# Kernel tuning notes

Measured on AMD Instinct MI355X. Metric: run time of the kernel, lower is better.

The kernel has to match this reference:

```python
import jax, jax.numpy as jnp
import numpy as np

N0, N1, N2 = 200000, 50000, 10000
D_IN, D_PROMPT, D_HID, D_OUT = 128, 64, 256, 2
E0, E1 = 800000, 160000


def _glorot(key, shape):
    fan_in, fan_out = shape[0], shape[1]
    lim = np.sqrt(6.0 / (fan_in + fan_out))
    return jax.random.uniform(key, shape, jnp.float32, -lim, lim)


def setup_inputs() -> dict:
    key = jax.random.key(0)
    ks = jax.random.split(key, 20)
    inp = {
        "features": jax.random.normal(ks[0], (N0, D_IN), jnp.float32),
        "membership_mask": jax.random.randint(ks[1], (N0,), 0, 2) > 0,
        "src0": jax.random.randint(ks[2], (E0,), 0, N0),
        "dst0": jax.random.randint(ks[3], (E0,), 0, N1),
        "src1": jax.random.randint(ks[4], (E1,), 0, N1),
        "dst1": jax.random.randint(ks[5], (E1,), 0, N2),
        "output_nodes_indices": jax.random.randint(ks[6], (N2,), 0, N2),
        # prompt MLPs
        "w_pin": _glorot(ks[7], (D_IN, D_PROMPT)),
        "b_pin": jnp.zeros((D_PROMPT,), jnp.float32),
        "w_pout": _glorot(ks[8], (D_IN, D_PROMPT)),
        "b_pout": jnp.zeros((D_PROMPT,), jnp.float32),
        # SAGEConv layer 0: (D_IN+D_PROMPT) -> D_HID
        "w_self0": _glorot(ks[9], (D_IN + D_PROMPT, D_HID)),
        "w_neigh0": _glorot(ks[10], (D_IN + D_PROMPT, D_HID)),
        "b0": jnp.zeros((D_HID,), jnp.float32),
        # SAGEConv layer 1: D_HID -> D_HID
        "w_self1": _glorot(ks[11], (D_HID, D_HID)),
        "w_neigh1": _glorot(ks[12], (D_HID, D_HID)),
        "b1": jnp.zeros((D_HID,), jnp.float32),
        # classifier
        "w_cls": _glorot(ks[13], (D_HID, D_OUT)),
        "b_cls": jnp.zeros((D_OUT,), jnp.float32),
    }
    return inp


def _sage_mean(h, src, dst, n_dst, w_self, w_neigh, b):
    # mean-aggregate src features into dst buckets (zero-degree -> 0, DGL semantics)
    agg = jax.ops.segment_sum(h[src], dst, num_segments=n_dst)
    deg = jax.ops.segment_sum(jnp.ones((src.shape[0],), h.dtype), dst, num_segments=n_dst)
    agg = agg / jnp.maximum(deg, 1.0)[:, None]
    return h[:n_dst] @ w_self + agg @ w_neigh + b


def reference(features, membership_mask, src0, dst0, src1, dst1, output_nodes_indices,
              w_pin, b_pin, w_pout, b_pout,
              w_self0, w_neigh0, b0, w_self1, w_neigh1, b1, w_cls, b_cls):
    p_in = jax.nn.relu(features @ w_pin + b_pin)
    p_out = jax.nn.relu(features @ w_pout + b_pout)
    sel = jnp.where(membership_mask[:, None], p_in, p_out)
    h = jnp.concatenate([features, sel], axis=1)          # [N0, D_IN+D_PROMPT]
    h = jax.nn.relu(_sage_mean(h, src0, dst0, N1, w_self0, w_neigh0, b0))  # [N1, D_HID]
    h = _sage_mean(h, src1, dst1, N2, w_self1, w_neigh1, b1)               # [N2, D_HID]
    logits = h @ w_cls + b_cls                             # [N2, D_OUT]
    return logits
```

## Files before the change

kernel.cpp:

```cpp
#include <hip/hip_runtime.h>


#define N0v 200000
#define N1v 50000
#define N2v 10000
#define E0v 800000
#define E1v 160000
#define TB0 49
#define TB1 10
#define TBL (TB0 + TB1)

using u16 = unsigned short;
typedef __attribute__((ext_vector_type(8))) short short8;
typedef __attribute__((ext_vector_type(4))) float f32x4;

__device__ __forceinline__ float b2f(u16 u) {
    union { unsigned int i; float f; } v; v.i = ((unsigned int)u) << 16; return v.f;
}
__device__ __forceinline__ u16 f2b(float f) {
    union { float f; unsigned int i; } v; v.f = f;
    return (u16)((v.i + 0x7fffu + ((v.i >> 16) & 1u)) >> 16);
}
__device__ __forceinline__ void split2(float f, u16& h, u16& l) {
    h = f2b(f);
    l = f2b(f - b2f(h));
}

__global__ void k_prep(const unsigned* mask, int* flag,
                       const float* w_pin, const float* w_pout, u16* WTph, u16* WTpl,
                       const float* ws0, const float* wn0, u16* WT0h, u16* WT0l,
                       const float* ws1, const float* wn1, u16* WT1h, u16* WT1l,
                       const float* bc, float* outp,
                       const int* __restrict__ dst0, const int* __restrict__ dst1,
                       int* cnt0, int* cnt1, int* rk0, int* rk1) {
    const int R0 = 50000;
    const int R1 = R0 + 128 * 128;
    const int R2 = R1 + 256 * 384;
    const int R3 = R2 + 256 * 512;
    const int R4 = R3 + 2 * N2v;
    const int R5 = R4 + E0v;
    const int R6 = R5 + E1v;
    for (int i = blockIdx.x * blockDim.x + threadIdx.x; i < R6;
         i += gridDim.x * blockDim.x) {
        if (i < R0) {
            if (mask[i] > 1u) atomicOr(flag, 1);
        } else if (i < R1) {
            int j = i - R0, n = j >> 7, k = j & 127;
            float f = (n < 64) ? w_pin[k * 64 + n] : w_pout[k * 64 + (n - 64)];
            split2(f, WTph[j], WTpl[j]);
        } else if (i < R2) {
            int j = i - R1, n = j / 384, k = j % 384;
            float f = (k < 192) ? ws0[k * 256 + n] : wn0[(k - 192) * 256 + n];
            split2(f, WT0h[j], WT0l[j]);
        } else if (i < R3) {
            int j = i - R2, n = j >> 9, k = j & 511;
            float f = (k < 256) ? ws1[k * 256 + n] : wn1[(k - 256) * 256 + n];
            split2(f, WT1h[j], WT1l[j]);
        } else if (i < R4) {
            int j = i - R3;
            outp[j] = bc[j & 1];
        } else if (i < R5) {
            int e = i - R4;
            rk0[e] = atomicAdd(&cnt0[dst0[e]], 1);
        } else {
            int e = i - R5;
            rk1[e] = atomicAdd(&cnt1[dst1[e]], 1);
        }
    }
}

__global__ __launch_bounds__(256) void k_scan_a(const int* __restrict__ cnt0,
                                                int* __restrict__ off0,
                                                const int* __restrict__ cnt1,
                                                int* __restrict__ off1,
                                                int* __restrict__ tsum) {
    __shared__ int sd[256];
    const int t = threadIdx.x;
    const int blk = blockIdx.x;
    const int g1 = (blk >= TB0);
    const int b = g1 ? blk - TB0 : blk;
    const int n = g1 ? N2v : N1v;
    const int* cnt = g1 ? cnt1 : cnt0;
    int* off = g1 ? off1 : off0;
    const int i0 = b * 1024 + t * 4;
    int c[4] = {0, 0, 0, 0};
    if (i0 + 3 < n) {
        *(int4*)c = *(const int4*)&cnt[i0];
    } else {
        for (int j = 0; j < 4; j++) if (i0 + j < n) c[j] = cnt[i0 + j];
    }
    int s = c[0] + c[1] + c[2] + c[3];
    sd[t] = s;
    __syncthreads();
#pragma unroll
    for (int d = 1; d < 256; d <<= 1) {
        int v = (t >= d) ? sd[t - d] : 0;
        __syncthreads();
        sd[t] += v;
        __syncthreads();
    }
    int run = sd[t] - s;
    int o4[4];
#pragma unroll
    for (int j = 0; j < 4; j++) { o4[j] = run; run += c[j]; }
    if (i0 + 3 < n) *(int4*)&off[i0] = *(const int4*)o4;
    else for (int j = 0; j < 4; j++) if (i0 + j < n) off[i0 + j] = o4[j];
    if (t == 255) tsum[blk] = sd[255];
}

__global__ __launch_bounds__(256) void k_scan_c(int* __restrict__ off0,
                                                int* __restrict__ off1,
                                                const int* __restrict__ tsum) {
    __shared__ int lbase;
    const int t = threadIdx.x;
    const int blk = blockIdx.x;
    const int g1 = (blk >= TB0);
    const int b = g1 ? blk - TB0 : blk;
    const int n = g1 ? N2v : N1v;
    int* off = g1 ? off1 : off0;
    if (t < 64) {
        int v = (t < TBL) ? tsum[t] : 0;
        int incl = v;
#pragma unroll
        for (int d = 1; d < 64; d <<= 1) {
            int u = __shfl_up(incl, d);
            if (t >= d) incl += u;
        }
        int total0 = __shfl(incl, TB0 - 1);
        if (t == blk) lbase = (incl - v) - (g1 ? total0 : 0);
    }
    __syncthreads();
    const int base = lbase;
    const int i0 = b * 1024 + t * 4;
    if (i0 + 3 < n) {
        int4 v = *(int4*)&off[i0];
        v.x += base; v.y += base; v.z += base; v.w += base;
        *(int4*)&off[i0] = v;
    } else {
        for (int j = 0; j < 4; j++) if (i0 + j < n) off[i0 + j] += base;
    }
    if (blk == 0 && t == 0) { off0[N1v] = E0v; off1[N2v] = E1v; }
}

__global__ __launch_bounds__(256) void k_scatter2(
    const int* __restrict__ src0, const int* __restrict__ dst0,
    const int* __restrict__ off0, const int* __restrict__ rk0, int* __restrict__ ei0,
    const int* __restrict__ src1, const int* __restrict__ dst1,
    const int* __restrict__ off1, const int* __restrict__ rk1, int* __restrict__ ei1) {
    const int part = blockIdx.x & 7;
    const int chunk = blockIdx.x >> 3;
    const int nch = gridDim.x >> 3;
    {
        const int per = (E0v + nch - 1) / nch;
        const int i1 = min((chunk + 1) * per, E0v);
        for (int i = chunk * per + (int)threadIdx.x; i < i1; i += 256) {
            int d = dst0[i];
            if (d / 6250 == part) ei0[off0[d] + rk0[i]] = src0[i];
        }
    }
    {
        const int per = (E1v + nch - 1) / nch;
        const int i1 = min((chunk + 1) * per, E1v);
        for (int i = chunk * per + (int)threadIdx.x; i < i1; i += 256) {
            int d = dst1[i];
            if (d / 1250 == part) ei1[off1[d] + rk1[i]] = src1[i];
        }
    }
}

__global__ __launch_bounds__(256, 4) void k_gemm_p(
    const float* __restrict__ A, const u16* __restrict__ Bh, const u16* __restrict__ Bl,
    const float* __restrict__ b_pin, const float* __restrict__ b_pout,
    const void* maskp, const int* __restrict__ flag, u16* __restrict__ G) {
    __shared__ __align__(16) u16 LA[8704];
    const int t = threadIdx.x;
    const int bm = blockIdx.x;
    const int lane = t & 63, w = t >> 6;
    const int m = lane & 15, q = lane >> 4;
    const int r0 = bm * 64;
    const int colbase = w * 32;

    const int fl = *flag;
    bool mk0, mk1;
    {
        const int ra = r0 + (t >> 3), rb = ra + 32;
        if (fl) {
            mk0 = ((const unsigned char*)maskp)[ra] != 0;
            mk1 = ((const unsigned char*)maskp)[rb] != 0;
        } else {
            mk0 = ((const int*)maskp)[ra] != 0;
            mk1 = ((const int*)maskp)[rb] != 0;
        }
    }

    const int r15 = t >> 4, ch = t & 15;
    uint4 h8r[4];
    {
        const int k0 = ch >> 2, q2 = ch & 3;
        const float* ap = &A[(size_t)(r0 + r15) * 128 + ch * 8];
        float4 va[8];
#pragma unroll
        for (int p = 0; p < 4; p++) {
            va[2 * p]     = *(const float4*)(ap + (size_t)p * 16 * 128);
            va[2 * p + 1] = *(const float4*)(ap + (size_t)p * 16 * 128 + 4);
        }
#pragma unroll
        for (int p = 0; p < 4; p++) {
            u16 h8[8];
            h8[0] = f2b(va[2 * p].x); h8[1] = f2b(va[2 * p].y);
            h8[2] = f2b(va[2 * p].z); h8[3] = f2b(va[2 * p].w);
            h8[4] = f2b(va[2 * p + 1].x); h8[5] = f2b(va[2 * p + 1].y);
            h8[6] = f2b(va[2 * p + 1].z); h8[7] = f2b(va[2 * p + 1].w);
            h8r[p] = *(const uint4*)h8;
            *(uint4*)&LA[((p * 4 + k0) * 66 + 16 * q2 + r15) * 8] = h8r[p];
        }
    }
    __syncthreads();

    const size_t ba = (size_t)(colbase + m) * 128 + q * 8;
    const size_t bb = (size_t)(colbase + 16 + m) * 128 + q * 8;

    f32x4 acc[4][2] = {};
#pragma unroll
    for (int k0 = 0; k0 < 4; k0++) {
        short8 b0h = *(const short8*)&Bh[ba + k0 * 32];
        short8 b0l = *(const short8*)&Bl[ba + k0 * 32];
        short8 b1h = *(const short8*)&Bh[bb + k0 * 32];
        short8 b1l = *(const short8*)&Bl[bb + k0 * 32];
#pragma unroll
        for (int mi = 0; mi < 4; mi++) {
            short8 af = *(const short8*)&LA[((mi * 4 + k0) * 66 + lane) * 8];
            acc[mi][0] = __builtin_amdgcn_mfma_f32_16x16x32_bf16(af, b0h, acc[mi][0], 0, 0, 0);
            acc[mi][0] = __builtin_amdgcn_mfma_f32_16x16x32_bf16(af, b0l, acc[mi][0], 0, 0, 0);
            acc[mi][1] = __builtin_amdgcn_mfma_f32_16x16x32_bf16(af, b1h, acc[mi][1], 0, 0, 0);
            acc[mi][1] = __builtin_amdgcn_mfma_f32_16x16x32_bf16(af, b1l, acc[mi][1], 0, 0, 0);
        }
    }

    float bv[2];
#pragma unroll
    for (int nt = 0; nt < 2; nt++) {
        int col = colbase + nt * 16 + m;
        bv[nt] = (col < 64) ? b_pin[col] : b_pout[col - 64];
    }
    __syncthreads();
#pragma unroll
    for (int mi = 0; mi < 4; mi++)
#pragma unroll
        for (int nt = 0; nt < 2; nt++)
#pragma unroll
            for (int r = 0; r < 4; r++) {
                float v = acc[mi][nt][r] + bv[nt];
                v = v > 0.f ? v : 0.f;
                LA[(mi * 16 + q * 4 + r) * 136 + colbase + nt * 16 + m] = f2b(v);
            }
    __syncthreads();
    {
        const int c8 = t & 7;
        const int rt = t >> 3;
        *(uint4*)&G[(size_t)(r0 + rt) * 192 + 128 + c8 * 8] =
            *(const uint4*)&LA[rt * 136 + (mk0 ? 0 : 64) + c8 * 8];
        *(uint4*)&G[(size_t)(r0 + 32 + rt) * 192 + 128 + c8 * 8] =
            *(const uint4*)&LA[(32 + rt) * 136 + (mk1 ? 0 : 64) + c8 * 8];
    }
#pragma unroll
    for (int p = 0; p < 4; p++) {
        *(uint4*)&G[(size_t)(r0 + r15 + 16 * p) * 192 + ch * 8] = h8r[p];
    }
}

template <int MODE, int KT, int SEGA0, int MT>
__global__ __launch_bounds__(256, 3) void k_g(
    const u16* __restrict__ A0, int s0, const u16* __restrict__ A1, int s1,
    const u16* __restrict__ Bh, const u16* __restrict__ Bl,
    const float* __restrict__ bias,
    u16* __restrict__ CH, float* __restrict__ outp, const float* __restrict__ wc,
    int M) {
    constexpr int MI = MT / 16;
    __shared__ __align__(16) u16 LA[MI * KT * 66 * 8];
    const int t = threadIdx.x;
    const int bm = blockIdx.x >> 1, bn = blockIdx.x & 1;
    const int lane = t & 63, w = t >> 6;
    const int m = lane & 15, q = lane >> 4;
    const int r0 = bm * MT;
    const int colbase = bn * 128 + w * 32;
    const int K = KT * 32;

    {
        constexpr int TPR = 256 / MT;
        constexpr int SPT = KT / TPR;
        const int rr = t / TPR, sub = t & (TPR - 1);
        int arow = r0 + rr; if (arow >= M) arow = M - 1;
        const int mi = rr >> 4, r15 = rr & 15;
#pragma unroll
        for (int s = 0; s < SPT; s++) {
            const int kc = sub * SPT + s;
#pragma unroll
            for (int q2 = 0; q2 < 4; q2++) {
                const int c = kc * 32 + q2 * 8;
                uint4 v = (c < SEGA0)
                              ? *(const uint4*)&A0[(size_t)arow * s0 + c]
                              : *(const uint4*)&A1[(size_t)arow * s1 + (c - SEGA0)];
                *(uint4*)&LA[((mi * KT + kc) * 66 + 16 * q2 + r15) * 8] = v;
            }
        }
    }
    __syncthreads();

    const size_t ba = (size_t)(colbase + m) * K + q * 8;
    const size_t bb = (size_t)(colbase + 16 + m) * K + q * 8;

    f32x4 acc[MI][2] = {};
#pragma unroll 1
    for (int kb = 0; kb < KT; kb += 4) {
#pragma unroll
        for (int k0 = 0; k0 < 4; k0++) {
            const size_t ko = (size_t)(kb + k0) * 32;
            short8 b0h = *(const short8*)&Bh[ba + ko];
            short8 b0l = *(const short8*)&Bl[ba + ko];
            short8 b1h = *(const short8*)&Bh[bb + ko];
            short8 b1l = *(const short8*)&Bl[bb + ko];
#pragma unroll
            for (int mi = 0; mi < MI; mi++) {
                short8 af = *(const short8*)&LA[((mi * KT + kb + k0) * 66 + lane) * 8];
                acc[mi][0] = __builtin_amdgcn_mfma_f32_16x16x32_bf16(af, b0h, acc[mi][0], 0, 0, 0);
                acc[mi][0] = __builtin_amdgcn_mfma_f32_16x16x32_bf16(af, b0l, acc[mi][0], 0, 0, 0);
                acc[mi][1] = __builtin_amdgcn_mfma_f32_16x16x32_bf16(af, b1h, acc[mi][1], 0, 0, 0);
                acc[mi][1] = __builtin_amdgcn_mfma_f32_16x16x32_bf16(af, b1l, acc[mi][1], 0, 0, 0);
            }
        }
    }

    if (MODE == 1) {
        float bv[2];
#pragma unroll
        for (int nt = 0; nt < 2; nt++) bv[nt] = bias[colbase + nt * 16 + m];
        __syncthreads();
#pragma unroll
        for (int mi = 0; mi < MI; mi++)
#pragma unroll
            for (int nt = 0; nt < 2; nt++)
#pragma unroll
                for (int r = 0; r < 4; r++) {
                    float v = acc[mi][nt][r] + bv[nt];
                    v = v > 0.f ? v : 0.f;
                    LA[(mi * 16 + q * 4 + r) * 136 + w * 32 + nt * 16 + m] = f2b(v);
                }
        __syncthreads();
        const int c16 = t & 15;
#pragma unroll
        for (int pass = 0; pass < MT / 16; pass++) {
            const int rt = pass * 16 + (t >> 4);
            const int row = r0 + rt;
            if (row < M) {
                *(uint4*)&CH[(size_t)row * 256 + bn * 128 + c16 * 8] =
                    *(const uint4*)&LA[rt * 136 + c16 * 8];
            }
        }
    } else {
        const int ca = colbase + m, cb = colbase + 16 + m;
        const float bva = bias[ca], bvb = bias[cb];
        const float w0a = wc[ca * 2], w1a = wc[ca * 2 + 1];
        const float w0b = wc[cb * 2], w1b = wc[cb * 2 + 1];
#pragma unroll
        for (int mi = 0; mi < MI; mi++) {
#pragma unroll
            for (int r = 0; r < 4; r++) {
                int row = r0 + mi * 16 + q * 4 + r;
                float va = acc[mi][0][r] + bva;
                float vb = acc[mi][1][r] + bvb;
                float p0 = va * w0a + vb * w0b;
                float p1 = va * w1a + vb * w1b;
#pragma unroll
                for (int s = 1; s < 16; s <<= 1) {
                    p0 += __shfl_xor(p0, s);
                    p1 += __shfl_xor(p1, s);
                }
                if (m == 0 && row < M) {
                    atomicAdd(&outp[row * 2], p0);
                    atomicAdd(&outp[row * 2 + 1], p1);
                }
            }
        }
    }
}

__global__ void k_agg0(const u16* __restrict__ G, const int* __restrict__ off,
                       const int* __restrict__ eidx, u16* __restrict__ aggH) {
    int wid = (blockIdx.x * blockDim.x + threadIdx.x) >> 6;
    int lane = threadIdx.x & 63;
    if (wid >= N1v) return;
    int b = off[wid], e = off[wid + 1];
    float f0 = 0.f, f1 = 0.f, p0 = 0.f;
    for (int base = b; base < e; base += 64) {
        int li = base + lane;
        int idx = eidx[li < e ? li : (e - 1)];
        int nch = e - base; if (nch > 64) nch = 64;
        int j = 0;
        for (; j + 4 <= nch; j += 4) {
            int sa = __shfl(idx, j), sb = __shfl(idx, j + 1);
            int sc = __shfl(idx, j + 2), sd = __shfl(idx, j + 3);
            const u16* ra = &G[(size_t)sa * 192];
            const u16* rb = &G[(size_t)sb * 192];
            const u16* rc = &G[(size_t)sc * 192];
            const u16* rd = &G[(size_t)sd * 192];
            unsigned fa = *(const unsigned*)&ra[2 * lane];
            unsigned fb = *(const unsigned*)&rb[2 * lane];
            unsigned fc = *(const unsigned*)&rc[2 * lane];
            unsigned fd = *(const unsigned*)&rd[2 * lane];
            u16 pa = ra[128 + lane], pb = rb[128 + lane];
            u16 pc = rc[128 + lane], pd = rd[128 + lane];
            f0 += b2f((u16)fa) + b2f((u16)fb) + b2f((u16)fc) + b2f((u16)fd);
            f1 += b2f((u16)(fa >> 16)) + b2f((u16)(fb >> 16)) +
                  b2f((u16)(fc >> 16)) + b2f((u16)(fd >> 16));
            p0 += b2f(pa) + b2f(pb) + b2f(pc) + b2f(pd);
        }
        for (; j < nch; j++) {
            int s = __shfl(idx, j);
            const u16* row = &G[(size_t)s * 192];
            unsigned fv = *(const unsigned*)&row[2 * lane];
            f0 += b2f((u16)fv);
            f1 += b2f((u16)(fv >> 16));
            p0 += b2f(row[128 + lane]);
        }
    }
    int deg = e - b;
    float inv = 1.0f / (float)(deg > 1 ? deg : 1);
    size_t rb2 = (size_t)wid * 192;
    *(unsigned*)&aggH[rb2 + 2 * lane] =
        (unsigned)f2b(f0 * inv) | ((unsigned)f2b(f1 * inv) << 16);
    aggH[rb2 + 128 + lane] = f2b(p0 * inv);
}

__global__ void k_agg1(const u16* __restrict__ h1H, const int* __restrict__ off,
                       const int* __restrict__ eidx, u16* __restrict__ aggH) {
    int wid = (blockIdx.x * blockDim.x + threadIdx.x) >> 6;
    int lane = threadIdx.x & 63;
    if (wid >= N2v) return;
    int b = off[wid], e = off[wid + 1];
    float a0 = 0.f, a1 = 0.f, a2 = 0.f, a3 = 0.f;
    for (int base = b; base < e; base += 64) {
        int li = base + lane;
        int idx = eidx[li < e ? li : (e - 1)];
        int nch = e - base; if (nch > 64) nch = 64;
        int j = 0;
        for (; j + 4 <= nch; j += 4) {
            int sa = __shfl(idx, j), sb = __shfl(idx, j + 1);
            int sc = __shfl(idx, j + 2), sd = __shfl(idx, j + 3);
            const u16* ra = &h1H[(size_t)sa * 256];
            const u16* rb = &h1H[(size_t)sb * 256];
            const u16* rc = &h1H[(size_t)sc * 256];
            const u16* rd = &h1H[(size_t)sd * 256];
            unsigned va0 = *(const unsigned*)&ra[2 * lane];
            unsigned vb0 = *(const unsigned*)&rb[2 * lane];
            unsigned vc0 = *(const unsigned*)&rc[2 * lane];
            unsigned vd0 = *(const unsigned*)&rd[2 * lane];
            unsigned va1 = *(const unsigned*)&ra[128 + 2 * lane];
            unsigned vb1 = *(const unsigned*)&rb[128 + 2 * lane];
            unsigned vc1 = *(const unsigned*)&rc[128 + 2 * lane];
            unsigned vd1 = *(const unsigned*)&rd[128 + 2 * lane];
            a0 += b2f((u16)va0) + b2f((u16)vb0) + b2f((u16)vc0) + b2f((u16)vd0);
            a1 += b2f((u16)(va0 >> 16)) + b2f((u16)(vb0 >> 16)) +
                  b2f((u16)(vc0 >> 16)) + b2f((u16)(vd0 >> 16));
            a2 += b2f((u16)va1) + b2f((u16)vb1) + b2f((u16)vc1) + b2f((u16)vd1);
            a3 += b2f((u16)(va1 >> 16)) + b2f((u16)(vb1 >> 16)) +
                  b2f((u16)(vc1 >> 16)) + b2f((u16)(vd1 >> 16));
        }
        for (; j < nch; j++) {
            int s = __shfl(idx, j);
            const u16* row = &h1H[(size_t)s * 256];
            unsigned v0 = *(const unsigned*)&row[2 * lane];
            unsigned v1 = *(const unsigned*)&row[128 + 2 * lane];
            a0 += b2f((u16)v0); a1 += b2f((u16)(v0 >> 16));
            a2 += b2f((u16)v1); a3 += b2f((u16)(v1 >> 16));
        }
    }
    int deg = e - b;
    float inv = 1.0f / (float)(deg > 1 ? deg : 1);
    size_t rb2 = (size_t)wid * 256;
    *(unsigned*)&aggH[rb2 + 2 * lane] =
        (unsigned)f2b(a0 * inv) | ((unsigned)f2b(a1 * inv) << 16);
    *(unsigned*)&aggH[rb2 + 128 + 2 * lane] =
        (unsigned)f2b(a2 * inv) | ((unsigned)f2b(a3 * inv) << 16);
}

extern "C" void kernel_launch(void* const* d_in, const int* in_sizes, int n_in,
                              void* d_out, int out_size, void* d_ws, size_t ws_size,
                              hipStream_t stream) {
    const float* features = (const float*)d_in[0];
    const void* maskp     = d_in[1];
    const int* src0       = (const int*)d_in[2];
    const int* dst0       = (const int*)d_in[3];
    const int* src1       = (const int*)d_in[4];
    const int* dst1       = (const int*)d_in[5];
    const float* w_pin    = (const float*)d_in[7];
    const float* b_pin    = (const float*)d_in[8];
    const float* w_pout   = (const float*)d_in[9];
    const float* b_pout   = (const float*)d_in[10];
    const float* w_self0  = (const float*)d_in[11];
    const float* w_neigh0 = (const float*)d_in[12];
    const float* b0       = (const float*)d_in[13];
    const float* w_self1  = (const float*)d_in[14];
    const float* w_neigh1 = (const float*)d_in[15];
    const float* b1       = (const float*)d_in[16];
    const float* w_cls    = (const float*)d_in[17];
    const float* b_cls    = (const float*)d_in[18];
    float* out = (float*)d_out;
    (void)in_sizes; (void)n_in; (void)out_size; (void)ws_size;

    char* ws = (char*)d_ws;
    size_t o = 0;
    auto alloc = [&](size_t bytes) { size_t r = o; o += (bytes + 255) & ~(size_t)255; return r; };
    size_t o_flag = alloc(4);
    size_t o_cnt0 = alloc(N1v * 4);
    size_t o_cnt1 = alloc(N2v * 4);
    size_t zero_end = o;
    size_t o_G    = alloc((size_t)N0v * 192 * 2);
    size_t o_aggH = alloc((size_t)N1v * 192 * 2);
    size_t o_h1H  = alloc((size_t)N1v * 256 * 2);
    size_t o_ag1H = alloc((size_t)N2v * 256 * 2);
    size_t o_wtph = alloc(128 * 128 * 2), o_wtpl = alloc(128 * 128 * 2);
    size_t o_wt0h = alloc(256 * 384 * 2), o_wt0l = alloc(256 * 384 * 2);
    size_t o_wt1h = alloc(256 * 512 * 2), o_wt1l = alloc(256 * 512 * 2);
    size_t o_off0 = alloc((N1v + 1) * 4);
    size_t o_off1 = alloc((N2v + 1) * 4);
    size_t o_ei0  = alloc((size_t)E0v * 4);
    size_t o_ei1  = alloc((size_t)E1v * 4);
    size_t o_rk0  = alloc((size_t)E0v * 4);
    size_t o_rk1  = alloc((size_t)E1v * 4);
    size_t o_tsum = alloc(TBL * 4);

    int* flag = (int*)(ws + o_flag);
    int* cnt0 = (int*)(ws + o_cnt0);
    int* cnt1 = (int*)(ws + o_cnt1);
    u16* G     = (u16*)(ws + o_G);
    u16* aggH  = (u16*)(ws + o_aggH);
    u16* h1H   = (u16*)(ws + o_h1H);
    u16* ag1H  = (u16*)(ws + o_ag1H);
    u16* WTph = (u16*)(ws + o_wtph);
    u16* WTpl = (u16*)(ws + o_wtpl);
    u16* WT0h = (u16*)(ws + o_wt0h);
    u16* WT0l = (u16*)(ws + o_wt0l);
    u16* WT1h = (u16*)(ws + o_wt1h);
    u16* WT1l = (u16*)(ws + o_wt1l);
    int* off0 = (int*)(ws + o_off0);
    int* off1 = (int*)(ws + o_off1);
    int* ei0  = (int*)(ws + o_ei0);
    int* ei1  = (int*)(ws + o_ei1);
    int* rk0  = (int*)(ws + o_rk0);
    int* rk1  = (int*)(ws + o_rk1);
    int* tsum = (int*)(ws + o_tsum);

    hipMemsetAsync(ws + o_flag, 0, zero_end - o_flag, stream);

    k_prep<<<1024, 256, 0, stream>>>((const unsigned*)maskp, flag,
                                     w_pin, w_pout, WTph, WTpl,
                                     w_self0, w_neigh0, WT0h, WT0l,
                                     w_self1, w_neigh1, WT1h, WT1l,
                                     b_cls, out, dst0, dst1, cnt0, cnt1, rk0, rk1);

    k_scan_a<<<TBL, 256, 0, stream>>>(cnt0, off0, cnt1, off1, tsum);
    k_scan_c<<<TBL, 256, 0, stream>>>(off0, off1, tsum);

    k_scatter2<<<2048, 256, 0, stream>>>(src0, dst0, off0, rk0, ei0,
                                         src1, dst1, off1, rk1, ei1);

    k_gemm_p<<<N0v / 64, 256, 0, stream>>>(features, WTph, WTpl,
                                           b_pin, b_pout, maskp, flag, G);

    k_agg0<<<(N1v + 3) / 4, 256, 0, stream>>>(G, off0, ei0, aggH);

    k_g<1, 12, 192, 64><<<((N1v + 63) / 64) * 2, 256, 0, stream>>>(
        G, 192, aggH, 192, WT0h, WT0l, b0, h1H, nullptr, nullptr, N1v);

    k_agg1<<<(N2v + 3) / 4, 256, 0, stream>>>(h1H, off1, ei1, ag1H);

    k_g<3, 16, 256, 32><<<((N2v + 31) / 32) * 2, 256, 0, stream>>>(
        h1H, 256, ag1H, 256, WT1h, WT1l, b1, nullptr, out, w_cls, N2v);
}
```

Baseline: 425.0 us.

## Make prompt GEMM persistent with register-resident weights and prefetched A tiles

Turns the prompt-MLP GEMM kernel into a persistent kernel with a fixed grid of 512 blocks, each looping over 64-row tiles. The bf16 hi/lo weight fragments and biases are now loaded into registers once per block instead of once per tile. While the current tile is computed, the next tile's fp32 features are prefetched into registers, and tiles alternate between two LDS staging buffers. This trades occupancy (launch bounds lowered to 2) and some tail imbalance across blocks for less repeated weight loading and overlap of global loads with MFMA work.

```diff
diff --git a/kernel.cpp b/kernel.cpp
--- a/kernel.cpp
+++ b/kernel.cpp
@@ -9,6 +9,8 @@
 #define TB0 49
 #define TB1 10
 #define TBL (TB0 + TB1)
+#define NTILE 3125
+#define PGRID 512
 
 using u16 = unsigned short;
 typedef __attribute__((ext_vector_type(8))) short short8;
@@ -168,42 +170,51 @@
     }
 }
 
-__global__ __launch_bounds__(256, 4) void k_gemm_p(
+__global__ __launch_bounds__(256, 2) void k_gemm_p(
     const float* __restrict__ A, const u16* __restrict__ Bh, const u16* __restrict__ Bl,
     const float* __restrict__ b_pin, const float* __restrict__ b_pout,
     const void* maskp, const int* __restrict__ flag, u16* __restrict__ G) {
-    __shared__ __align__(16) u16 LA[8704];
+    __shared__ __align__(16) u16 STG[2][8448];
+    __shared__ __align__(16) u16 EPI[8704];
     const int t = threadIdx.x;
-    const int bm = blockIdx.x;
     const int lane = t & 63, w = t >> 6;
     const int m = lane & 15, q = lane >> 4;
-    const int r0 = bm * 64;
     const int colbase = w * 32;
-
+    const int r15 = t >> 4, ch = t & 15;
+    const int k0s = ch >> 2, q2s = ch & 3;
+
+    const size_t ba = (size_t)(colbase + m) * 128 + q * 8;
+    const size_t bb = (size_t)(colbase + 16 + m) * 128 + q * 8;
+    short8 BfA[4][2], BfB[4][2];
+#pragma unroll
+    for (int k0 = 0; k0 < 4; k0++) {
+        BfA[k0][0] = *(const short8*)&Bh[ba + k0 * 32];
+        BfA[k0][1] = *(const short8*)&Bl[ba + k0 * 32];
+        BfB[k0][0] = *(const short8*)&Bh[bb + k0 * 32];
+        BfB[k0][1] = *(const short8*)&Bl[bb + k0 * 32];
+    }
     const int fl = *flag;
-    bool mk0, mk1;
+    float bv0, bv1;
     {
-        const int ra = r0 + (t >> 3), rb = ra + 32;
-        if (fl) {
-            mk0 = ((const unsigned char*)maskp)[ra] != 0;
-            mk1 = ((const unsigned char*)maskp)[rb] != 0;
-        } else {
-            mk0 = ((const int*)maskp)[ra] != 0;
-            mk1 = ((const int*)maskp)[rb] != 0;
-        }
-    }
-
-    const int r15 = t >> 4, ch = t & 15;
-    uint4 h8r[4];
+        int c0 = colbase + m, c1 = colbase + 16 + m;
+        bv0 = (c0 < 64) ? b_pin[c0] : b_pout[c0 - 64];
+        bv1 = (c1 < 64) ? b_pin[c1] : b_pout[c1 - 64];
+    }
+
+    float4 va[8];
     {
-        const int k0 = ch >> 2, q2 = ch & 3;
-        const float* ap = &A[(size_t)(r0 + r15) * 128 + ch * 8];
-        float4 va[8];
+        const float* ap = &A[(size_t)(blockIdx.x * 64 + r15) * 128 + ch * 8];
 #pragma unroll
         for (int p = 0; p < 4; p++) {
             va[2 * p]     = *(const float4*)(ap + (size_t)p * 16 * 128);
             va[2 * p + 1] = *(const float4*)(ap + (size_t)p * 16 * 128 + 4);
         }
+    }
+
+    int buf = 0;
+    for (int bm = blockIdx.x; bm < NTILE; bm += PGRID, buf ^= 1) {
+        const int r0 = bm * 64;
+        u16* stg = STG[buf];
 #pragma unroll
         for (int p = 0; p < 4; p++) {
             u16 h8[8];
@@ -211,61 +222,69 @@
             h8[2] = f2b(va[2 * p].z); h8[3] = f2b(va[2 * p].w);
             h8[4] = f2b(va[2 * p + 1].x); h8[5] = f2b(va[2 * p + 1].y);
             h8[6] = f2b(va[2 * p + 1].z); h8[7] = f2b(va[2 * p + 1].w);
-            h8r[p] = *(const uint4*)h8;
-            *(uint4*)&LA[((p * 4 + k0) * 66 + 16 * q2 + r15) * 8] = h8r[p];
-        }
-    }
-    __syncthreads();
-
-    const size_t ba = (size_t)(colbase + m) * 128 + q * 8;
-    const size_t bb = (size_t)(colbase + 16 + m) * 128 + q * 8;
-
-    f32x4 acc[4][2] = {};
-#pragma unroll
-    for (int k0 = 0; k0 < 4; k0++) {
-        short8 b0h = *(const short8*)&Bh[ba + k0 * 32];
-        short8 b0l = *(const short8*)&Bl[ba + k0 * 32];
-        short8 b1h = *(const short8*)&Bh[bb + k0 * 32];
-        short8 b1l = *(const short8*)&Bl[bb + k0 * 32];
-#pragma unroll
-        for (int mi = 0; mi < 4; mi++) {
-            short8 af = *(const short8*)&LA[((mi * 4 + k0) * 66 + lane) * 8];
-            acc[mi][0] = __builtin_amdgcn_mfma_f32_16x16x32_bf16(af, b0h, acc[mi][0], 0, 0, 0);
-            acc[mi][0] = __builtin_amdgcn_mfma_f32_16x16x32_bf16(af, b0l, acc[mi][0], 0, 0, 0);
-            acc[mi][1] = __builtin_amdgcn_mfma_f32_16x16x32_bf16(af, b1h, acc[mi][1], 0, 0, 0);
-            acc[mi][1] = __builtin_amdgcn_mfma_f32_16x16x32_bf16(af, b1l, acc[mi][1], 0, 0, 0);
-        }
-    }
-
-    float bv[2];
-#pragma unroll
-    for (int nt = 0; nt < 2; nt++) {
-        int col = colbase + nt * 16 + m;
-        bv[nt] = (col < 64) ? b_pin[col] : b_pout[col - 64];
-    }
-    __syncthreads();
-#pragma unroll
-    for (int mi = 0; mi < 4; mi++)
-#pragma unroll
-        for (int nt = 0; nt < 2; nt++)
+            *(uint4*)&stg[((p * 4 + k0s) * 66 + 16 * q2s + r15) * 8] = *(const uint4*)h8;
+        }
+        __syncthreads();
+
+        if (bm + PGRID < NTILE) {
+            const float* ap = &A[(size_t)((bm + PGRID) * 64 + r15) * 128 + ch * 8];
+#pragma unroll
+            for (int p = 0; p < 4; p++) {
+                va[2 * p]     = *(const float4*)(ap + (size_t)p * 16 * 128);
+                va[2 * p + 1] = *(const float4*)(ap + (size_t)p * 16 * 128 + 4);
+            }
+        }
+        bool mk0, mk1;
+        {
+            const int ra = r0 + (t >> 3), rb = ra + 32;
+            if (fl) {
+                mk0 = ((const unsigned char*)maskp)[ra] != 0;
+                mk1 = ((const unsigned char*)maskp)[rb] != 0;
+            } else {
+                mk0 = ((const int*)maskp)[ra] != 0;
+                mk1 = ((const int*)maskp)[rb] != 0;
+            }
+        }
+
+        f32x4 acc[4][2] = {};
+#pragma unroll
+        for (int k0 = 0; k0 < 4; k0++) {
+#pragma unroll
+            for (int mi = 0; mi < 4; mi++) {
+                short8 af = *(const short8*)&stg[((mi * 4 + k0) * 66 + lane) * 8];
+                acc[mi][0] = __builtin_amdgcn_mfma_f32_16x16x32_bf16(af, BfA[k0][0], acc[mi][0], 0, 0, 0);
+                acc[mi][0] = __builtin_amdgcn_mfma_f32_16x16x32_bf16(af, BfA[k0][1], acc[mi][0], 0, 0, 0);
+                acc[mi][1] = __builtin_amdgcn_mfma_f32_16x16x32_bf16(af, BfB[k0][0], acc[mi][1], 0, 0, 0);
+                acc[mi][1] = __builtin_amdgcn_mfma_f32_16x16x32_bf16(af, BfB[k0][1], acc[mi][1], 0, 0, 0);
+            }
+        }
+
+#pragma unroll
+        for (int mi = 0; mi < 4; mi++)
 #pragma unroll
             for (int r = 0; r < 4; r++) {
-                float v = acc[mi][nt][r] + bv[nt];
-                v = v > 0.f ? v : 0.f;
-                LA[(mi * 16 + q * 4 + r) * 136 + colbase + nt * 16 + m] = f2b(v);
-            }
-    __syncthreads();
-    {
-        const int c8 = t & 7;
-        const int rt = t >> 3;
-        *(uint4*)&G[(size_t)(r0 + rt) * 192 + 128 + c8 * 8] =
-            *(const uint4*)&LA[rt * 136 + (mk0 ? 0 : 64) + c8 * 8];
-        *(uint4*)&G[(size_t)(r0 + 32 + rt) * 192 + 128 + c8 * 8] =
-            *(const uint4*)&LA[(32 + rt) * 136 + (mk1 ? 0 : 64) + c8 * 8];
-    }
-#pragma unroll
-    for (int p = 0; p < 4; p++) {
-        *(uint4*)&G[(size_t)(r0 + r15 + 16 * p) * 192 + ch * 8] = h8r[p];
+                float v0 = acc[mi][0][r] + bv0;
+                float v1 = acc[mi][1][r] + bv1;
+                v0 = v0 > 0.f ? v0 : 0.f;
+                v1 = v1 > 0.f ? v1 : 0.f;
+                EPI[(mi * 16 + q * 4 + r) * 136 + colbase + m] = f2b(v0);
+                EPI[(mi * 16 + q * 4 + r) * 136 + colbase + 16 + m] = f2b(v1);
+            }
+        __syncthreads();
+
+        {
+            const int c8 = t & 7;
+            const int rt = t >> 3;
+            *(uint4*)&G[(size_t)(r0 + rt) * 192 + 128 + c8 * 8] =
+                *(const uint4*)&EPI[rt * 136 + (mk0 ? 0 : 64) + c8 * 8];
+            *(uint4*)&G[(size_t)(r0 + 32 + rt) * 192 + 128 + c8 * 8] =
+                *(const uint4*)&EPI[(32 + rt) * 136 + (mk1 ? 0 : 64) + c8 * 8];
+        }
+#pragma unroll
+        for (int p = 0; p < 4; p++) {
+            uint4 v = *(const uint4*)&stg[((p * 4 + k0s) * 66 + 16 * q2s + r15) * 8];
+            *(uint4*)&G[(size_t)(r0 + r15 + 16 * p) * 192 + ch * 8] = v;
+        }
     }
 }
 
@@ -565,8 +584,8 @@
     k_scatter2<<<2048, 256, 0, stream>>>(src0, dst0, off0, rk0, ei0,
                                          src1, dst1, off1, rk1, ei1);
 
-    k_gemm_p<<<N0v / 64, 256, 0, stream>>>(features, WTph, WTpl,
-                                           b_pin, b_pout, maskp, flag, G);
+    k_gemm_p<<<PGRID, 256, 0, stream>>>(features, WTph, WTpl,
+                                        b_pin, b_pout, maskp, flag, G);
 
     k_agg0<<<(N1v + 3) / 4, 256, 0, stream>>>(G, off0, ei0, aggH);
 
```

Measured after the change: 413.2 us. 1.03x faster.
